# Optimization experiments

Hardware: AMD Instinct MI355X
Metric: run time of the kernel (lower is better)

Reference implementation:

```python
import jax, jax.numpy as jnp
import numpy as np

B, L, D, N = 32, 2048, 1024, 16
N_ITERS = 4
EPS = 1e-8
RMS_EPS = 1e-6
H = 2 * D  # SwiGLU hidden


def setup_inputs() -> dict:
    key = jax.random.key(0)
    ks = jax.random.split(key, 16)
    w = lambda i, shape: jax.random.normal(ks[i], shape, dtype=jnp.float32) * 0.02
    return {
        "encoder_output": jax.random.normal(ks[0], (B, L, D), dtype=jnp.float32),
        "slots_noise": jax.random.normal(ks[1], (B, N, D), dtype=jnp.float32),
        "slots_mu": w(2, (1, 1, D)),
        "slots_sigma": jnp.abs(w(3, (1, 1, D))),
        "g_in": jnp.ones((D,), jnp.float32),     # norm_input.weight
        "g_slots": jnp.ones((D,), jnp.float32),  # norm_slots.weight
        "Wq": w(4, (D, D)),   # torch Linear weight layout (out, in)
        "Wk": w(5, (D, D)),
        "Wv": w(6, (D, D)),
        "w1": w(7, (H, D)),
        "w2": w(8, (H, D)),
        "w3": w(9, (D, H)),
        "W_ih": w(10, (3 * D, D)),  # GRUCell weight_ih (r,z,n stacked)
        "W_hh": w(11, (3 * D, D)),
        "b_ih": jnp.zeros((3 * D,), jnp.float32),
        "b_hh": jnp.zeros((3 * D,), jnp.float32),
    }


def _rmsnorm(x, g):
    var = jnp.mean(x * x, axis=-1, keepdims=True)
    return x * jax.lax.rsqrt(var + RMS_EPS) * g


def _gru_cell(x, h, W_ih, W_hh, b_ih, b_hh):
    # torch.nn.GRUCell: gates ordered (r, z, n)
    gi = x @ W_ih.T + b_ih   # [..., 3D]
    gh = h @ W_hh.T + b_hh
    gi_r, gi_z, gi_n = jnp.split(gi, 3, axis=-1)
    gh_r, gh_z, gh_n = jnp.split(gh, 3, axis=-1)
    r = jax.nn.sigmoid(gi_r + gh_r)
    z = jax.nn.sigmoid(gi_z + gh_z)
    n = jnp.tanh(gi_n + r * gh_n)
    return (1.0 - z) * n + z * h


def reference(encoder_output, slots_noise, slots_mu, slots_sigma, g_in, g_slots,
              Wq, Wk, Wv, w1, w2, w3, W_ih, W_hh, b_ih, b_hh):
    d = encoder_output.shape[-1]
    scale = d ** (-0.5)

    inputs = _rmsnorm(encoder_output, g_in)          # [B, L, D]
    k = inputs @ Wk.T                                # [B, L, D]
    v = inputs @ Wv.T                                # [B, L, D]

    slots = slots_mu + slots_sigma * slots_noise     # [B, N, D]

    for _ in range(N_ITERS):
        slots_prev = slots
        s = _rmsnorm(slots, g_slots)                 # [B, N, D]
        q = s @ Wq.T                                 # [B, N, D]
        dots = jnp.einsum('bnd,bld->bnl', q, k) * scale   # [B, N, L]
        attn = jax.nn.softmax(dots, axis=1)          # competitive softmax over slots
        updates = jnp.einsum('bnl,bld->bnd', attn + EPS, v)     # [B, N, D]
        updates = updates / (jnp.sum(attn, axis=-1, keepdims=True) + EPS)
        # SwiGLU
        updates = (jax.nn.silu(updates @ w1.T) * (updates @ w2.T)) @ w3.T
        slots = _gru_cell(updates, slots_prev, W_ih, W_hh, b_ih, b_hh)
    return slots
```

## Files before the change

### kernel.cpp

```cpp
#include <hip/hip_runtime.h>
#include <hip/hip_bf16.h>
#include <stdint.h>


typedef __bf16 bf16;
typedef __bf16 bf16x4 __attribute__((ext_vector_type(4)));
typedef __bf16 bf16x8 __attribute__((ext_vector_type(8)));
typedef float  f32x4  __attribute__((ext_vector_type(4)));

#define MFMA16(a,b,c) __builtin_amdgcn_mfma_f32_16x16x32_bf16((a),(b),(c),0,0,0)

__device__ __forceinline__ void gload16(const void* g, void* l) {
  __builtin_amdgcn_global_load_lds((__attribute__((address_space(1))) const void*)g,
                                   (__attribute__((address_space(3))) void*)l, 16, 0, 0);
}

template<int OUT_F32>
__device__ __forceinline__ void g64(const bf16* __restrict__ A, const bf16* __restrict__ B,
                                    void* __restrict__ C, int N, int K,
                                    int brow, int bcol, bf16* As, bf16* Bs)
{
  const int tid = threadIdx.x, wave = tid >> 6, lane = tid & 63;
  const int wm = wave >> 1, wn = wave & 1;
  const int r8 = lane >> 3, c8 = (lane & 7) * 8;
  const int cl = lane & 15, rh = lane >> 4;
  f32x4 acc[2][2] = {};

  const bf16* pa0 = A + (size_t)(brow + wave * 16 + r8) * K + c8;
  const bf16* pa1 = A + (size_t)(brow + wave * 16 + 8 + r8) * K + c8;
  const bf16* pb0 = B + (size_t)(bcol + wave * 16 + r8) * K + c8;
  const bf16* pb1 = B + (size_t)(bcol + wave * 16 + 8 + r8) * K + c8;

  auto ST = [&](int T) {
    const int k0 = T * 64, s = T % 3;
    gload16(pa0 + k0, As + s * 4096 + (wave * 16) * 64);
    gload16(pa1 + k0, As + s * 4096 + (wave * 16 + 8) * 64);
    gload16(pb0 + k0, Bs + s * 4096 + (wave * 16) * 64);
    gload16(pb1 + k0, Bs + s * 4096 + (wave * 16 + 8) * 64);
  };

  const int nt = K >> 6;
  ST(0);
  ST(1);
#pragma unroll 3
  for (int t = 0; t < nt; ++t) {
    __builtin_amdgcn_s_barrier();
    if (t + 2 < nt) {
      ST(t + 2);
      asm volatile("s_waitcnt vmcnt(8)" ::: "memory");
    } else if (t + 1 < nt) {
      asm volatile("s_waitcnt vmcnt(4)" ::: "memory");
    } else {
      asm volatile("s_waitcnt vmcnt(0)" ::: "memory");
    }
    __builtin_amdgcn_sched_barrier(0);
    __builtin_amdgcn_s_barrier();
    const int s = t % 3;
#pragma unroll
    for (int kk = 0; kk < 2; ++kk) {
      bf16x8 af[2], bfv[2];
#pragma unroll
      for (int m = 0; m < 2; ++m)
        af[m] = *(const bf16x8*)(As + s * 4096 + (wm * 32 + m * 16 + cl) * 64 + kk * 32 + rh * 8);
#pragma unroll
      for (int n = 0; n < 2; ++n)
        bfv[n] = *(const bf16x8*)(Bs + s * 4096 + (wn * 32 + n * 16 + cl) * 64 + kk * 32 + rh * 8);
#pragma unroll
      for (int m = 0; m < 2; ++m)
#pragma unroll
        for (int n = 0; n < 2; ++n)
          acc[m][n] = MFMA16(af[m], bfv[n], acc[m][n]);
    }
  }

#pragma unroll
  for (int m = 0; m < 2; ++m)
#pragma unroll
    for (int n = 0; n < 2; ++n) {
      int row0 = brow + wm * 32 + m * 16 + rh * 4;
      int col  = bcol + wn * 32 + n * 16 + cl;
#pragma unroll
      for (int r = 0; r < 4; ++r) {
        if (OUT_F32) ((float*)C)[(size_t)(row0 + r) * N + col] = acc[m][n][r];
        else         ((bf16*)C)[(size_t)(row0 + r) * N + col] = (bf16)acc[m][n][r];
      }
    }
}

template<int OUT_F32>
__global__ __launch_bounds__(256, 3)
void gemm_bt64(const bf16* __restrict__ A0, const bf16* __restrict__ B0, void* __restrict__ C0,
               const bf16* __restrict__ A1, const bf16* __restrict__ B1, void* __restrict__ C1,
               int N, int K0, int K1, float* zbuf)
{
  __shared__ __align__(16) bf16 As[3 * 4096];
  __shared__ __align__(16) bf16 Bs[3 * 4096];
  if (zbuf != nullptr && blockIdx.x == 0 && blockIdx.y == 0 && blockIdx.z == 0) {
    zbuf[threadIdx.x] = 0.f;
    zbuf[threadIdx.x + 256] = 0.f;
  }
  const bf16* A = blockIdx.z ? A1 : A0;
  const bf16* B = blockIdx.z ? B1 : B0;
  void* C = blockIdx.z ? C1 : C0;
  const int K = blockIdx.z ? K1 : K0;
  g64<OUT_F32>(A, B, C, N, K, blockIdx.y * 64, blockIdx.x * 64, As, Bs);
}

__global__ __launch_bounds__(256, 3)
void gemm_pre(const bf16* __restrict__ wkT, const bf16* __restrict__ wqT, bf16* __restrict__ qm_w,
              const bf16* __restrict__ w12, const bf16* __restrict__ wvT, bf16* __restrict__ w12v,
              const bf16* __restrict__ wih, const bf16* __restrict__ w3T, bf16* __restrict__ wih3)
{
  __shared__ __align__(16) bf16 As[3 * 4096];
  __shared__ __align__(16) bf16 Bs[3 * 4096];
  const int id = blockIdx.x;
  if (id < 256)       g64<0>(wkT, wqT, qm_w, 1024, 1024, (id >> 4) * 64, (id & 15) * 64, As, Bs);
  else if (id < 1280) { int t = id - 256;  g64<0>(w12, wvT, w12v, 1024, 1024, (t >> 4) * 64, (t & 15) * 64, As, Bs); }
  else                { int t = id - 1280; g64<0>(wih, w3T, wih3, 2048, 1024, (t >> 5) * 64, (t & 31) * 64, As, Bs); }
}

__global__ __launch_bounds__(256, 3)
void gemm_swiglu(const bf16* __restrict__ A, const bf16* __restrict__ B12, bf16* __restrict__ G)
{
  __shared__ __align__(16) bf16 As[2][64 * 64];
  __shared__ __align__(16) bf16 B1s[2][64 * 64];
  __shared__ __align__(16) bf16 B2s[2][64 * 64];
  const int tid = threadIdx.x, wave = tid >> 6, lane = tid & 63;
  const int wm = wave >> 1, wn = wave & 1;
  const int brow = blockIdx.y * 64, bcol = blockIdx.x * 64;
  const int r8 = lane >> 3, c8 = (lane & 7) * 8;
  const int cl = lane & 15, rh = lane >> 4;
  f32x4 acc1[2][2] = {}, acc2[2][2] = {};

  const bf16* pa0 = A   + (size_t)(brow + wave * 16 + r8) * 1024 + c8;
  const bf16* pa1 = A   + (size_t)(brow + wave * 16 + 8 + r8) * 1024 + c8;
  const bf16* p10 = B12 + (size_t)(bcol + wave * 16 + r8) * 1024 + c8;
  const bf16* p11 = B12 + (size_t)(bcol + wave * 16 + 8 + r8) * 1024 + c8;
  const bf16* p20 = B12 + (size_t)(2048 + bcol + wave * 16 + r8) * 1024 + c8;
  const bf16* p21 = B12 + (size_t)(2048 + bcol + wave * 16 + 8 + r8) * 1024 + c8;

#define STSW(T) {                                                   \
    int k0_ = (T) * 64, s_ = (T) & 1;                               \
    gload16(pa0 + k0_, &As[s_][(wave * 16) * 64]);                  \
    gload16(pa1 + k0_, &As[s_][(wave * 16 + 8) * 64]);              \
    gload16(p10 + k0_, &B1s[s_][(wave * 16) * 64]);                 \
    gload16(p11 + k0_, &B1s[s_][(wave * 16 + 8) * 64]);             \
    gload16(p20 + k0_, &B2s[s_][(wave * 16) * 64]);                 \
    gload16(p21 + k0_, &B2s[s_][(wave * 16 + 8) * 64]);             \
  }

  STSW(0)
  for (int t = 0; t < 16; ++t) {
    if (t < 15) {
      STSW(t + 1)
      asm volatile("s_waitcnt vmcnt(6)" ::: "memory");
    } else {
      asm volatile("s_waitcnt vmcnt(0)" ::: "memory");
    }
    __builtin_amdgcn_sched_barrier(0);
    __builtin_amdgcn_s_barrier();
    __builtin_amdgcn_sched_barrier(0);
    const int s = t & 1;
#pragma unroll
    for (int kk = 0; kk < 2; ++kk) {
      bf16x8 af[2], b1v[2], b2v[2];
#pragma unroll
      for (int m = 0; m < 2; ++m)
        af[m] = *(const bf16x8*)&As[s][(wm * 32 + m * 16 + cl) * 64 + kk * 32 + rh * 8];
#pragma unroll
      for (int n = 0; n < 2; ++n) {
        b1v[n] = *(const bf16x8*)&B1s[s][(wn * 32 + n * 16 + cl) * 64 + kk * 32 + rh * 8];
        b2v[n] = *(const bf16x8*)&B2s[s][(wn * 32 + n * 16 + cl) * 64 + kk * 32 + rh * 8];
      }
#pragma unroll
      for (int m = 0; m < 2; ++m)
#pragma unroll
        for (int n = 0; n < 2; ++n) {
          acc1[m][n] = MFMA16(af[m], b1v[n], acc1[m][n]);
          acc2[m][n] = MFMA16(af[m], b2v[n], acc2[m][n]);
        }
    }
    __builtin_amdgcn_sched_barrier(0);
    __builtin_amdgcn_s_barrier();
    __builtin_amdgcn_sched_barrier(0);
  }
#undef STSW

#pragma unroll
  for (int m = 0; m < 2; ++m)
#pragma unroll
    for (int n = 0; n < 2; ++n) {
      int row0 = brow + wm * 32 + m * 16 + rh * 4;
      int col  = bcol + wn * 32 + n * 16 + cl;
#pragma unroll
      for (int r = 0; r < 4; ++r) {
        float h1 = acc1[m][n][r], h2 = acc2[m][n][r];
        G[(size_t)(row0 + r) * 2048 + col] = (bf16)(h1 / (1.f + __expf(-h1)) * h2);
      }
    }
}

__global__ __launch_bounds__(256, 2)
void fused_attn(const bf16* __restrict__ qm, const bf16* __restrict__ x,
                bf16* __restrict__ part, float* __restrict__ attn_sum)
{
  extern __shared__ __align__(16) char smem[];
  char* ss  = smem;
  char* ksl = smem + 32768;
  float* p_lds = (float*)(smem + 65536);

  const int lc = blockIdx.x, b = blockIdx.y;
  const int tid = threadIdx.x, wave = tid >> 6, lane = tid & 63;
  const int cl = lane & 15, rh = lane >> 4;

  const bf16* sb = qm + (size_t)b * 16 * 1024;
  {
    const int c16 = tid & 127, row2 = tid >> 7;
#pragma unroll
    for (int i = 0; i < 8; ++i) {
      int row = i * 2 + row2;
      int colb = (c16 * 16) ^ ((row & 7) << 4);
      gload16(sb + row * 1024 + colb / 2, ss + i * 4096 + wave * 1024);
    }
  }

  const bf16* kb = x + ((size_t)b * 2048 + lc * 128) * 1024;
  const int ksw  = ((lane & 7) ^ ((lane >> 3) & 7)) * 8;
  const int krow = wave * 8 + (lane >> 3);

#define STAGE_KS(KT) {                                                            \
    char* d_ = ksl + ((KT) & 1) * 16384;                                          \
    _Pragma("unroll")                                                             \
    for (int i = 0; i < 4; ++i)                                                   \
      gload16(kb + (size_t)(i * 32 + krow) * 1024 + (KT) * 64 + ksw,              \
              d_ + (i * 32 + wave * 8) * 128);                                    \
  }

  f32x4 acc[2] = {};
  STAGE_KS(0)
  for (int kt = 0; kt < 16; ++kt) {
    if (kt < 15) { STAGE_KS(kt + 1) }
    __builtin_amdgcn_sched_barrier(0);
    if (kt < 15) asm volatile("s_waitcnt vmcnt(4)" ::: "memory");
    else         asm volatile("s_waitcnt vmcnt(0)" ::: "memory");
    __builtin_amdgcn_sched_barrier(0);
    __builtin_amdgcn_s_barrier();
    const char* sbuf = ksl + (kt & 1) * 16384;
#pragma unroll
    for (int kk = 0; kk < 2; ++kk) {
      bf16x8 af = *(const bf16x8*)(ss + cl * 2048 +
                    ((kt * 128 + kk * 64 + rh * 16) ^ ((cl & 7) << 4)));
#pragma unroll
      for (int n = 0; n < 2; ++n) {
        int row = wave * 32 + n * 16 + cl;
        bf16x8 bfv = *(const bf16x8*)(sbuf + row * 128 +
                      ((kk * 64 + rh * 16) ^ ((row & 7) << 4)));
        acc[n] = MFMA16(af, bfv, acc[n]);
      }
    }
    __builtin_amdgcn_s_barrier();
    __builtin_amdgcn_sched_barrier(0);
  }
#undef STAGE_KS

  const float scale = 0.03125f;
  float rs[4] = {0.f, 0.f, 0.f, 0.f};
#pragma unroll
  for (int n = 0; n < 2; ++n) {
    float xv[4];
#pragma unroll
    for (int r = 0; r < 4; ++r) xv[r] = acc[n][r] * scale;
    float mx = fmaxf(fmaxf(xv[0], xv[1]), fmaxf(xv[2], xv[3]));
    mx = fmaxf(mx, __shfl_xor(mx, 16));
    mx = fmaxf(mx, __shfl_xor(mx, 32));
    float e[4], sm = 0.f;
#pragma unroll
    for (int r = 0; r < 4; ++r) { e[r] = __expf(xv[r] - mx); sm += e[r]; }
    sm += __shfl_xor(sm, 16);
    sm += __shfl_xor(sm, 32);
    float inv = 1.f / sm;
    f32x4 pk;
#pragma unroll
    for (int r = 0; r < 4; ++r) { float av = e[r] * inv; rs[r] += av; pk[r] = av; }
    int ll = wave * 32 + n * 16 + cl;
    *(f32x4*)&p_lds[ll * 20 + rh * 4] = pk;
  }
#pragma unroll
  for (int off = 1; off < 16; off <<= 1) {
#pragma unroll
    for (int r = 0; r < 4; ++r) rs[r] += __shfl_xor(rs[r], off);
  }
  if (cl == 0) {
#pragma unroll
    for (int r = 0; r < 4; ++r) atomicAdd(&attn_sum[b * 16 + rh * 4 + r], rs[r]);
  }
  __syncthreads();

  const bf16* vb = x + ((size_t)b * 2048 + lc * 128) * 1024 + tid * 4;
  float pacc[16][4] = {};
  for (int l = 0; l < 128; ++l) {
    bf16x4 vv = *(const bf16x4*)(vb + (size_t)l * 1024);
    float vf0 = (float)vv[0], vf1 = (float)vv[1], vf2 = (float)vv[2], vf3 = (float)vv[3];
    float pv[16];
    *(f32x4*)&pv[0]  = *(const f32x4*)&p_lds[l * 20];
    *(f32x4*)&pv[4]  = *(const f32x4*)&p_lds[l * 20 + 4];
    *(f32x4*)&pv[8]  = *(const f32x4*)&p_lds[l * 20 + 8];
    *(f32x4*)&pv[12] = *(const f32x4*)&p_lds[l * 20 + 12];
#pragma unroll
    for (int n = 0; n < 16; ++n) {
      pacc[n][0] += pv[n] * vf0; pacc[n][1] += pv[n] * vf1;
      pacc[n][2] += pv[n] * vf2; pacc[n][3] += pv[n] * vf3;
    }
  }
  bf16* pb = part + ((size_t)(lc * 32 + b) * 16) * 1024 + tid * 4;
#pragma unroll
  for (int n = 0; n < 16; ++n) {
    bf16x4 o;
#pragma unroll
    for (int r = 0; r < 4; ++r) o[r] = (bf16)pacc[n][r];
    *(bf16x4*)(pb + (size_t)n * 1024) = o;
  }
}

__global__ void updates_finalize(const bf16* __restrict__ part, const float* __restrict__ attn_sum,
                                 bf16* __restrict__ updraw)
{
  int idx8 = (blockIdx.x * 256 + threadIdx.x) * 8;
  int m = idx8 >> 10;
  float s[8] = {};
#pragma unroll
  for (int ls = 0; ls < 16; ++ls) {
    bf16x8 v = *(const bf16x8*)(part + idx8 + (size_t)ls * 524288);
#pragma unroll
    for (int j = 0; j < 8; ++j) s[j] += (float)v[j];
  }
  float inv = 1.f / (attn_sum[m] + 1e-8f);
  bf16x8 o;
#pragma unroll
  for (int j = 0; j < 8; ++j) o[j] = (bf16)(s[j] * inv);
  *(bf16x8*)(updraw + idx8) = o;
}

__global__ __launch_bounds__(256)
void gru_pw_fused(const float* __restrict__ gi, const float* __restrict__ gh,
                  const float* __restrict__ bih, const float* __restrict__ bhh,
                  const float* __restrict__ g_sl,
                  float* __restrict__ slots, bf16* __restrict__ slots_bf,
                  bf16* __restrict__ s_bf, float* __restrict__ outp)
{
  const int m = blockIdx.x, tid = threadIdx.x;
  const int d0 = tid * 4;
  const size_t base = (size_t)m * 3072 + d0;
  f32x4 gir = *(const f32x4*)(gi + base),        ghr = *(const f32x4*)(gh + base);
  f32x4 giz = *(const f32x4*)(gi + base + 1024), ghz = *(const f32x4*)(gh + base + 1024);
  f32x4 gin = *(const f32x4*)(gi + base + 2048), ghn = *(const f32x4*)(gh + base + 2048);
  f32x4 br  = *(const f32x4*)(bih + d0),        bhr = *(const f32x4*)(bhh + d0);
  f32x4 bz  = *(const f32x4*)(bih + 1024 + d0), bhz = *(const f32x4*)(bhh + 1024 + d0);
  f32x4 bn  = *(const f32x4*)(bih + 2048 + d0), bhn = *(const f32x4*)(bhh + 2048 + d0);
  f32x4 h   = *(const f32x4*)(slots + (size_t)m * 1024 + d0);
  float o[4]; float ssum = 0.f;
#pragma unroll
  for (int j = 0; j < 4; ++j) {
    float r  = gir[j] + br[j] + ghr[j] + bhr[j];
    float z  = giz[j] + bz[j] + ghz[j] + bhz[j];
    float nn = gin[j] + bn[j];
    float hn = ghn[j] + bhn[j];
    r = 1.f / (1.f + expf(-r));
    z = 1.f / (1.f + expf(-z));
    nn = tanhf(nn + r * hn);
    o[j] = (1.f - z) * nn + z * h[j];
    ssum += o[j] * o[j];
  }
#pragma unroll
  for (int off = 32; off; off >>= 1) ssum += __shfl_xor(ssum, off);
  __shared__ float red[4];
  if ((tid & 63) == 0) red[tid >> 6] = ssum;
  __syncthreads();
  float tot = red[0] + red[1] + red[2] + red[3];
  float rsc = rsqrtf(tot * (1.f / 1024.f) + 1e-6f);
  f32x4 gv = *(const f32x4*)(g_sl + d0);
  f32x4 of; bf16x4 ob, sb;
#pragma unroll
  for (int j = 0; j < 4; ++j) { of[j] = o[j]; ob[j] = (bf16)o[j]; sb[j] = (bf16)(o[j] * rsc * gv[j]); }
  *(f32x4*)(slots + (size_t)m * 1024 + d0) = of;
  *(f32x4*)(outp  + (size_t)m * 1024 + d0) = of;
  *(bf16x4*)(slots_bf + (size_t)m * 1024 + d0) = ob;
  *(bf16x4*)(s_bf     + (size_t)m * 1024 + d0) = sb;
}

__global__ __launch_bounds__(256)
void init_slots_fused(const float* __restrict__ noise, const float* __restrict__ mu,
                      const float* __restrict__ sigma, const float* __restrict__ g_sl,
                      float* __restrict__ slots, bf16* __restrict__ slots_bf,
                      bf16* __restrict__ s_bf)
{
  const int m = blockIdx.x, tid = threadIdx.x;
  const int d0 = tid * 4;
  f32x4 nz = *(const f32x4*)(noise + (size_t)m * 1024 + d0);
  f32x4 mv = *(const f32x4*)(mu + d0);
  f32x4 sg = *(const f32x4*)(sigma + d0);
  float o[4]; float ssum = 0.f;
#pragma unroll
  for (int j = 0; j < 4; ++j) { o[j] = mv[j] + sg[j] * nz[j]; ssum += o[j] * o[j]; }
#pragma unroll
  for (int off = 32; off; off >>= 1) ssum += __shfl_xor(ssum, off);
  __shared__ float red[4];
  if ((tid & 63) == 0) red[tid >> 6] = ssum;
  __syncthreads();
  float tot = red[0] + red[1] + red[2] + red[3];
  float rsc = rsqrtf(tot * (1.f / 1024.f) + 1e-6f);
  f32x4 gv = *(const f32x4*)(g_sl + d0);
  f32x4 of; bf16x4 ob, sb;
#pragma unroll
  for (int j = 0; j < 4; ++j) { of[j] = o[j]; ob[j] = (bf16)o[j]; sb[j] = (bf16)(o[j] * rsc * gv[j]); }
  *(f32x4*)(slots + (size_t)m * 1024 + d0) = of;
  *(bf16x4*)(slots_bf + (size_t)m * 1024 + d0) = ob;
  *(bf16x4*)(s_bf     + (size_t)m * 1024 + d0) = sb;
}

__global__ __launch_bounds__(256)
void rmsnorm_cast(const float* __restrict__ x, const float* __restrict__ g, bf16* __restrict__ y)
{
  const int row = blockIdx.x, tid = threadIdx.x;
  float4 xv = ((const float4*)(x + (size_t)row * 1024))[tid];
  float ss = xv.x * xv.x + xv.y * xv.y + xv.z * xv.z + xv.w * xv.w;
#pragma unroll
  for (int off = 32; off; off >>= 1) ss += __shfl_xor(ss, off);
  __shared__ float red[4];
  if ((tid & 63) == 0) red[tid >> 6] = ss;
  __syncthreads();
  float tot = red[0] + red[1] + red[2] + red[3];
  float rs = rsqrtf(tot * (1.f / 1024.f) + 1e-6f);
  float4 gv = ((const float4*)g)[tid];
  bf16x4 o;
  o[0] = (bf16)(xv.x * rs * gv.x); o[1] = (bf16)(xv.y * rs * gv.y);
  o[2] = (bf16)(xv.z * rs * gv.z); o[3] = (bf16)(xv.w * rs * gv.w);
  *(bf16x4*)(y + (size_t)row * 1024 + tid * 4) = o;
}

__global__ __launch_bounds__(256)
void transpose_all(const float* __restrict__ Wq, const float* __restrict__ Wk,
                   const float* __restrict__ Wv, const float* __restrict__ w3,
                   bf16* __restrict__ wqT, bf16* __restrict__ wkT,
                   bf16* __restrict__ wvT, bf16* __restrict__ w3T)
{
  __shared__ float tile[32][33];
  const int z = blockIdx.z;
  const float* in; bf16* out; int R, C;
  if      (z == 0) { in = Wq; out = wqT; R = 1024; C = 1024; }
  else if (z == 1) { in = Wk; out = wkT; R = 1024; C = 1024; }
  else if (z == 2) { in = Wv; out = wvT; R = 1024; C = 1024; }
  else             { in = w3; out = w3T; R = 1024; C = 2048; }
  const int bx = blockIdx.x * 32, by = blockIdx.y * 32;
  if (bx >= C) return;
  const int tx = threadIdx.x & 31, ty = threadIdx.x >> 5;
#pragma unroll
  for (int i = 0; i < 32; i += 8)
    tile[ty + i][tx] = in[(size_t)(by + ty + i) * C + bx + tx];
  __syncthreads();
#pragma unroll
  for (int i = 0; i < 32; i += 8)
    out[(size_t)(bx + ty + i) * R + by + tx] = (bf16)tile[tx][ty + i];
}

__global__ void cast_all(const float* __restrict__ w1, const float* __restrict__ w2,
                         const float* __restrict__ Wih, const float* __restrict__ Whh,
                         bf16* __restrict__ w12_bf, bf16* __restrict__ wih_bf,
                         bf16* __restrict__ whh_b)
{
  int i = (blockIdx.x * 256 + threadIdx.x) * 4;
  const float* src; bf16* dst; int o;
  if      (i < 2097152)  { src = w1;  dst = w12_bf; o = i; }
  else if (i < 4194304)  { src = w2;  dst = w12_bf + 2097152; o = i - 2097152; }
  else if (i < 7340032)  { src = Wih; dst = wih_bf; o = i - 4194304; }
  else                   { src = Whh; dst = whh_b;  o = i - 7340032; }
  float4 v = *(const float4*)(src + o);
  bf16x4 ov; ov[0] = (bf16)v.x; ov[1] = (bf16)v.y; ov[2] = (bf16)v.z; ov[3] = (bf16)v.w;
  *(bf16x4*)(dst + o) = ov;
}

extern "C" void kernel_launch(void* const* d_in, const int* in_sizes, int n_in,
                              void* d_out, int out_size, void* d_ws, size_t ws_size,
                              hipStream_t stream)
{
  const float* enc    = (const float*)d_in[0];
  const float* noise  = (const float*)d_in[1];
  const float* mu     = (const float*)d_in[2];
  const float* sigma  = (const float*)d_in[3];
  const float* g_in   = (const float*)d_in[4];
  const float* g_sl   = (const float*)d_in[5];
  const float* Wq     = (const float*)d_in[6];
  const float* Wk     = (const float*)d_in[7];
  const float* Wv     = (const float*)d_in[8];
  const float* w1     = (const float*)d_in[9];
  const float* w2     = (const float*)d_in[10];
  const float* w3     = (const float*)d_in[11];
  const float* Wih    = (const float*)d_in[12];
  const float* Whh    = (const float*)d_in[13];
  const float* bih    = (const float*)d_in[14];
  const float* bhh    = (const float*)d_in[15];

  char* p = (char*)d_ws;
  auto alloc = [&](size_t bytes) { char* r = p; p += (bytes + 255) & ~(size_t)255; return (void*)r; };

  bf16* inputs  = (bf16*)alloc((size_t)32 * 2048 * 1024 * 2);
  bf16* qm_w    = (bf16*)alloc((size_t)1024 * 1024 * 2);
  bf16* wqT_b   = (bf16*)alloc((size_t)1024 * 1024 * 2);
  bf16* wkT_b   = (bf16*)alloc((size_t)1024 * 1024 * 2);
  bf16* wvT_b   = (bf16*)alloc((size_t)1024 * 1024 * 2);
  bf16* w3T_b   = (bf16*)alloc((size_t)2048 * 1024 * 2);
  bf16* w12_bf  = (bf16*)alloc((size_t)4096 * 1024 * 2);
  bf16* w12v    = (bf16*)alloc((size_t)4096 * 1024 * 2);
  bf16* wih_bf  = (bf16*)alloc((size_t)3072 * 1024 * 2);
  bf16* wih3_b  = (bf16*)alloc((size_t)3072 * 2048 * 2);
  bf16* whh_b   = (bf16*)alloc((size_t)3072 * 1024 * 2);
  float* slots  = (float*)alloc(512 * 1024 * 4);
  bf16* slots_bf= (bf16*)alloc(512 * 1024 * 2);
  bf16* s_bf    = (bf16*)alloc(512 * 1024 * 2);
  bf16* qm_bf   = (bf16*)alloc(512 * 1024 * 2);
  float* attn_sum = (float*)alloc(32 * 16 * 4);
  bf16* part    = (bf16*)alloc((size_t)16 * 512 * 1024 * 2);
  bf16* updraw  = (bf16*)alloc(512 * 1024 * 2);
  bf16* g_bf    = (bf16*)alloc((size_t)512 * 2048 * 2);
  float* gif    = (float*)alloc((size_t)512 * 3072 * 4);
  float* ghf    = (float*)alloc((size_t)512 * 3072 * 4);

  transpose_all<<<dim3(64, 32, 4), 256, 0, stream>>>(Wq, Wk, Wv, w3, wqT_b, wkT_b, wvT_b, w3T_b);
  cast_all<<<10240, 256, 0, stream>>>(w1, w2, Wih, Whh, w12_bf, wih_bf, whh_b);
  gemm_pre<<<2816, 256, 0, stream>>>(wkT_b, wqT_b, qm_w, w12_bf, wvT_b, w12v, wih_bf, w3T_b, wih3_b);

  rmsnorm_cast<<<65536, 256, 0, stream>>>(enc, g_in, inputs);
  init_slots_fused<<<512, 256, 0, stream>>>(noise, mu, sigma, g_sl, slots, slots_bf, s_bf);

  hipFuncSetAttribute(reinterpret_cast<const void*>(fused_attn),
                      hipFuncAttributeMaxDynamicSharedMemorySize, 75776);

  for (int it = 0; it < 4; ++it) {
    gemm_bt64<0><<<dim3(16, 8, 1), 256, 0, stream>>>(s_bf, qm_w, qm_bf, s_bf, qm_w, qm_bf,
                                                     1024, 1024, 1024, attn_sum);
    fused_attn<<<dim3(16, 32), 256, 75776, stream>>>(qm_bf, inputs, part, attn_sum);
    updates_finalize<<<256, 256, 0, stream>>>(part, attn_sum, updraw);
    gemm_swiglu<<<dim3(32, 8), 256, 0, stream>>>(updraw, w12v, g_bf);
    gemm_bt64<1><<<dim3(48, 8, 2), 256, 0, stream>>>(g_bf, wih3_b, gif, slots_bf, whh_b, ghf,
                                                     3072, 2048, 1024, nullptr);
    float* outp = (it == 3) ? (float*)d_out : slots;
    gru_pw_fused<<<512, 256, 0, stream>>>(gif, ghf, bih, bhh, g_sl, slots, slots_bf, s_bf, outp);
  }
}
```

Baseline: 689.8 us.

## Split P·V out of attention kernel into MFMA GEMM on pre-transposed inputs

The fused attention kernel now only computes the slot softmax and writes the bf16 probabilities P to global memory. A new pv_gemm kernel computes P·X with MFMA over a triple-buffered LDS pipeline, reading a one-time transposed copy of the normalized inputs, and applies the attn_sum normalization in its epilogue. This replaces the scalar FMA P·V loop, the 16-way partial buffer and the separate finalize kernel. In exchange it adds a large one-time transpose of the inputs (extra 128MB of traffic), an extra workspace buffer, and a re-read of X per iteration from the transposed copy.

```diff
diff --git a/kernel.cpp b/kernel.cpp
--- a/kernel.cpp
+++ b/kernel.cpp
@@ -202,12 +202,11 @@
 
 __global__ __launch_bounds__(256, 2)
 void fused_attn(const bf16* __restrict__ qm, const bf16* __restrict__ x,
-                bf16* __restrict__ part, float* __restrict__ attn_sum)
+                bf16* __restrict__ P, float* __restrict__ attn_sum)
 {
   extern __shared__ __align__(16) char smem[];
   char* ss  = smem;
   char* ksl = smem + 32768;
-  float* p_lds = (float*)(smem + 65536);
 
   const int lc = blockIdx.x, b = blockIdx.y;
   const int tid = threadIdx.x, wave = tid >> 6, lane = tid & 63;
@@ -279,11 +278,13 @@
     sm += __shfl_xor(sm, 16);
     sm += __shfl_xor(sm, 32);
     float inv = 1.f / sm;
-    f32x4 pk;
-#pragma unroll
-    for (int r = 0; r < 4; ++r) { float av = e[r] * inv; rs[r] += av; pk[r] = av; }
-    int ll = wave * 32 + n * 16 + cl;
-    *(f32x4*)&p_lds[ll * 20 + rh * 4] = pk;
+    int l = lc * 128 + wave * 32 + n * 16 + cl;
+#pragma unroll
+    for (int r = 0; r < 4; ++r) {
+      float av = e[r] * inv;
+      rs[r] += av;
+      P[((size_t)b * 16 + rh * 4 + r) * 2048 + l] = (bf16)av;
+    }
   }
 #pragma unroll
   for (int off = 1; off < 16; off <<= 1) {
@@ -294,51 +295,86 @@
 #pragma unroll
     for (int r = 0; r < 4; ++r) atomicAdd(&attn_sum[b * 16 + rh * 4 + r], rs[r]);
   }
+}
+
+__global__ __launch_bounds__(256, 4)
+void pv_gemm(const bf16* __restrict__ P, const bf16* __restrict__ xT,
+             const float* __restrict__ attn_sum, bf16* __restrict__ updraw)
+{
+  __shared__ __align__(16) bf16 Ap[3 * 1024];
+  __shared__ __align__(16) bf16 Bp[3 * 4096];
+  const int dt = blockIdx.x, b = blockIdx.y;
+  const int tid = threadIdx.x, wave = tid >> 6;
+  const int lane = tid & 63, cl = lane & 15, rh = lane >> 4;
+
+  const bf16* Pb = P  + (size_t)b * 16 * 2048;
+  const bf16* Xb = xT + ((size_t)b * 1024 + dt * 64) * 2048;
+  const int rrow = tid >> 3, rcol = (tid & 7) * 8;
+
+  auto ST = [&](int T) {
+    const int k0 = T * 64, s = T % 3;
+    gload16(Xb + (size_t)rrow * 2048 + k0 + rcol,        Bp + s * 4096 + wave * 512);
+    gload16(Xb + (size_t)(32 + rrow) * 2048 + k0 + rcol, Bp + s * 4096 + 2048 + wave * 512);
+    if (tid < 128)
+      gload16(Pb + (size_t)rrow * 2048 + k0 + rcol, Ap + s * 1024 + wave * 512);
+  };
+
+  f32x4 acc = {};
+  ST(0);
+  ST(1);
+#pragma unroll 3
+  for (int t = 0; t < 32; ++t) {
+    __builtin_amdgcn_s_barrier();
+    if (t + 2 < 32) {
+      ST(t + 2);
+      asm volatile("s_waitcnt vmcnt(4)" ::: "memory");
+    } else if (t + 1 < 32) {
+      asm volatile("s_waitcnt vmcnt(2)" ::: "memory");
+    } else {
+      asm volatile("s_waitcnt vmcnt(0)" ::: "memory");
+    }
+    __builtin_amdgcn_sched_barrier(0);
+    __builtin_amdgcn_s_barrier();
+    const int s = t % 3;
+#pragma unroll
+    for (int kk = 0; kk < 2; ++kk) {
+      bf16x8 af  = *(const bf16x8*)(Ap + s * 1024 + cl * 64 + kk * 32 + rh * 8);
+      bf16x8 bfv = *(const bf16x8*)(Bp + s * 4096 + (wave * 16 + cl) * 64 + kk * 32 + rh * 8);
+      acc = MFMA16(af, bfv, acc);
+    }
+  }
+
+  const int dcol = dt * 64 + wave * 16 + cl;
+#pragma unroll
+  for (int j = 0; j < 4; ++j) {
+    int slot = rh * 4 + j;
+    float inv = 1.f / (attn_sum[b * 16 + slot] + 1e-8f);
+    updraw[((size_t)b * 16 + slot) * 1024 + dcol] = (bf16)(acc[j] * inv);
+  }
+}
+
+__global__ __launch_bounds__(256)
+void transpose_x(const bf16* __restrict__ in, bf16* __restrict__ out)
+{
+  __shared__ bf16 tile[64][72];
+  const int l0 = blockIdx.x * 64, d0 = blockIdx.y * 64, b = blockIdx.z;
+  const int t = threadIdx.x;
+  const int r = t >> 3, c = (t & 7) * 8;
+#pragma unroll
+  for (int i = 0; i < 2; ++i) {
+    int row = i * 32 + r;
+    bf16x8 v = *(const bf16x8*)(in + ((size_t)(b * 2048 + l0 + row)) * 1024 + d0 + c);
+    *(bf16x8*)&tile[row][c] = v;
+  }
   __syncthreads();
-
-  const bf16* vb = x + ((size_t)b * 2048 + lc * 128) * 1024 + tid * 4;
-  float pacc[16][4] = {};
-  for (int l = 0; l < 128; ++l) {
-    bf16x4 vv = *(const bf16x4*)(vb + (size_t)l * 1024);
-    float vf0 = (float)vv[0], vf1 = (float)vv[1], vf2 = (float)vv[2], vf3 = (float)vv[3];
-    float pv[16];
-    *(f32x4*)&pv[0]  = *(const f32x4*)&p_lds[l * 20];
-    *(f32x4*)&pv[4]  = *(const f32x4*)&p_lds[l * 20 + 4];
-    *(f32x4*)&pv[8]  = *(const f32x4*)&p_lds[l * 20 + 8];
-    *(f32x4*)&pv[12] = *(const f32x4*)&p_lds[l * 20 + 12];
-#pragma unroll
-    for (int n = 0; n < 16; ++n) {
-      pacc[n][0] += pv[n] * vf0; pacc[n][1] += pv[n] * vf1;
-      pacc[n][2] += pv[n] * vf2; pacc[n][3] += pv[n] * vf3;
-    }
-  }
-  bf16* pb = part + ((size_t)(lc * 32 + b) * 16) * 1024 + tid * 4;
-#pragma unroll
-  for (int n = 0; n < 16; ++n) {
-    bf16x4 o;
-#pragma unroll
-    for (int r = 0; r < 4; ++r) o[r] = (bf16)pacc[n][r];
-    *(bf16x4*)(pb + (size_t)n * 1024) = o;
-  }
-}
-
-__global__ void updates_finalize(const bf16* __restrict__ part, const float* __restrict__ attn_sum,
-                                 bf16* __restrict__ updraw)
-{
-  int idx8 = (blockIdx.x * 256 + threadIdx.x) * 8;
-  int m = idx8 >> 10;
-  float s[8] = {};
-#pragma unroll
-  for (int ls = 0; ls < 16; ++ls) {
-    bf16x8 v = *(const bf16x8*)(part + idx8 + (size_t)ls * 524288);
-#pragma unroll
-    for (int j = 0; j < 8; ++j) s[j] += (float)v[j];
-  }
-  float inv = 1.f / (attn_sum[m] + 1e-8f);
-  bf16x8 o;
-#pragma unroll
-  for (int j = 0; j < 8; ++j) o[j] = (bf16)(s[j] * inv);
-  *(bf16x8*)(updraw + idx8) = o;
+#pragma unroll
+  for (int i = 0; i < 2; ++i) {
+    int drow = i * 32 + r;
+    bf16x8 o;
+#pragma unroll
+    for (int j = 0; j < 8; ++j) o[j] = tile[c + j][drow];
+    *(bf16x8*)(out + ((size_t)b * 1024 + d0 + drow) * 2048 + l0 + c) = o;
+  }
 }
 
 __global__ __launch_bounds__(256)
@@ -504,6 +540,7 @@
   auto alloc = [&](size_t bytes) { char* r = p; p += (bytes + 255) & ~(size_t)255; return (void*)r; };
 
   bf16* inputs  = (bf16*)alloc((size_t)32 * 2048 * 1024 * 2);
+  bf16* xT      = (bf16*)alloc((size_t)32 * 1024 * 2048 * 2);
   bf16* qm_w    = (bf16*)alloc((size_t)1024 * 1024 * 2);
   bf16* wqT_b   = (bf16*)alloc((size_t)1024 * 1024 * 2);
   bf16* wkT_b   = (bf16*)alloc((size_t)1024 * 1024 * 2);
@@ -519,7 +556,7 @@
   bf16* s_bf    = (bf16*)alloc(512 * 1024 * 2);
   bf16* qm_bf   = (bf16*)alloc(512 * 1024 * 2);
   float* attn_sum = (float*)alloc(32 * 16 * 4);
-  bf16* part    = (bf16*)alloc((size_t)16 * 512 * 1024 * 2);
+  bf16* Pbuf    = (bf16*)alloc((size_t)32 * 16 * 2048 * 2);
   bf16* updraw  = (bf16*)alloc(512 * 1024 * 2);
   bf16* g_bf    = (bf16*)alloc((size_t)512 * 2048 * 2);
   float* gif    = (float*)alloc((size_t)512 * 3072 * 4);
@@ -530,16 +567,17 @@
   gemm_pre<<<2816, 256, 0, stream>>>(wkT_b, wqT_b, qm_w, w12_bf, wvT_b, w12v, wih_bf, w3T_b, wih3_b);
 
   rmsnorm_cast<<<65536, 256, 0, stream>>>(enc, g_in, inputs);
+  transpose_x<<<dim3(32, 16, 32), 256, 0, stream>>>(inputs, xT);
   init_slots_fused<<<512, 256, 0, stream>>>(noise, mu, sigma, g_sl, slots, slots_bf, s_bf);
 
   hipFuncSetAttribute(reinterpret_cast<const void*>(fused_attn),
-                      hipFuncAttributeMaxDynamicSharedMemorySize, 75776);
+                      hipFuncAttributeMaxDynamicSharedMemorySize, 65536);
 
   for (int it = 0; it < 4; ++it) {
     gemm_bt64<0><<<dim3(16, 8, 1), 256, 0, stream>>>(s_bf, qm_w, qm_bf, s_bf, qm_w, qm_bf,
                                                      1024, 1024, 1024, attn_sum);
-    fused_attn<<<dim3(16, 32), 256, 75776, stream>>>(qm_bf, inputs, part, attn_sum);
-    updates_finalize<<<256, 256, 0, stream>>>(part, attn_sum, updraw);
+    fused_attn<<<dim3(16, 32), 256, 65536, stream>>>(qm_bf, inputs, Pbuf, attn_sum);
+    pv_gemm<<<dim3(16, 32), 256, 0, stream>>>(Pbuf, xT, attn_sum, updraw);
     gemm_swiglu<<<dim3(32, 8), 256, 0, stream>>>(updraw, w12v, g_bf);
     gemm_bt64<1><<<dim3(48, 8, 2), 256, 0, stream>>>(g_bf, wih3_b, gif, slots_bf, whh_b, ghf,
                                                      3072, 2048, 1024, nullptr);
```

Result: slower. 734.2 us (+6.4%).
